# Performance work log

Measured on AMD Instinct MI355X. Metric: run time of the kernel, lower is better.

Reference implementation:

```python
import jax, jax.numpy as jnp
import numpy as np

EPS = 1e-5
HEADS = 8
SR = 4


def bn(x, gamma, beta, mean, var):
    # BatchNorm in inference form; channel axis = 1
    shape = (1, -1) + (1,) * (x.ndim - 2)
    inv = gamma.reshape(shape) / jnp.sqrt(var.reshape(shape) + EPS)
    return (x - mean.reshape(shape)) * inv + beta.reshape(shape)


def setup_inputs() -> dict:
    key = jax.random.key(0)
    ks = jax.random.split(key, 8)
    B, C, H, W = 2, 256, 128, 128
    N = H * W
    conv1d_std = np.sqrt(2.0 / C)            # fan_out = 1*C
    conv2d_std = np.sqrt(2.0 / (SR * SR * C))  # fan_out = sr*sr*C
    return {
        "x": jax.random.normal(ks[0], (B, C, N), dtype=jnp.float32),
        "w_q": jax.random.normal(ks[1], (C, C), dtype=jnp.float32) * conv1d_std,
        "w_k": jax.random.normal(ks[2], (C, C), dtype=jnp.float32) * conv1d_std,
        "w_sr": jax.random.normal(ks[3], (C, C, SR, SR), dtype=jnp.float32) * conv2d_std,
        "sr_gamma": jnp.ones((C,), jnp.float32),
        "sr_beta": jnp.zeros((C,), jnp.float32),
        "sr_mean": jnp.zeros((C,), jnp.float32),
        "sr_var": jnp.ones((C,), jnp.float32),
        "w_proj": jax.random.normal(ks[4], (C, C), dtype=jnp.float32) * conv1d_std,
        "proj_gamma": jnp.ones((C,), jnp.float32),
        "proj_beta": jnp.zeros((C,), jnp.float32),
        "proj_mean": jnp.zeros((C,), jnp.float32),
        "proj_var": jnp.ones((C,), jnp.float32),
        "H": 128,
        "W": 128,
    }


def reference(x, w_q, w_k, w_sr, sr_gamma, sr_beta, sr_mean, sr_var,
              w_proj, proj_gamma, proj_beta, proj_mean, proj_var, H, W):
    B, C, N = x.shape
    hd = C // HEADS
    scale = hd ** -0.5
    # q: Conv1d(k=1) == channel matmul -> (B, heads, N, hd)
    q = jnp.einsum('oc,bcn->bon', w_q, x).reshape(B, HEADS, hd, N).transpose(0, 1, 3, 2)
    # spatial reduction: Conv2d(k=SR, s=SR) as patch-reshape + einsum, then BN
    xp = x.reshape(B, C, H // SR, SR, W // SR, SR)
    xr = jnp.einsum('bchpwq,ocpq->bohw', xp, w_sr).reshape(B, C, (H // SR) * (W // SR))
    xr = bn(xr, sr_gamma, sr_beta, sr_mean, sr_var)
    # k: (B, heads, hd, N_kv)
    k = jnp.einsum('oc,bcm->bom', w_k, xr).reshape(B, HEADS, hd, -1)
    # scores (B, heads, N, N_kv) -> max over kv
    scores = jnp.einsum('bhnd,bhdm->bhnm', q, k) * scale
    attn = scores.max(axis=-1)                # (B, heads, N)
    # v = mean-pooled x, identical per head -> matmul collapses to sum over heads
    v = x.mean(axis=-1)                       # (B, C)
    out = jnp.einsum('bhn,bc->bcn', attn, v)  # (B, C, N)
    out = jnp.einsum('oc,bcn->bon', w_proj, out)
    return bn(out, proj_gamma, proj_beta, proj_mean, proj_var)
```

## Files before the change

### kernel.cpp

```cpp
#include <hip/hip_runtime.h>
#include <hip/hip_bf16.h>
#include <math.h>

#define EPSF 1e-5f
#define SCALE 0.17677669529663687f

typedef __bf16 bf16x8 __attribute__((ext_vector_type(8)));
typedef __bf16 bf16x4 __attribute__((ext_vector_type(4)));
typedef float f32x4 __attribute__((ext_vector_type(4)));


__global__ __launch_bounds__(256) void k_wprep(const float* __restrict__ wq,
                                               const float* __restrict__ wk,
                                               const float* __restrict__ wsr,
                                               __bf16* __restrict__ wqf,
                                               __bf16* __restrict__ wkb,
                                               __bf16* __restrict__ wsrf,
                                               float* __restrict__ v,
                                               float* __restrict__ ssg) {
    int bi = blockIdx.x, t = threadIdx.x;
    if (bi >= 576) {
        int e = (bi - 576) * 256 + t;
        *(float4*)&ssg[e << 2] = make_float4(0.f, 0.f, 0.f, 0.f);
        return;
    }
    if (bi < 32) {
        if (bi == 0) { v[t] = 0.f; v[256 + t] = 0.f; }
        int tt = bi * 256 + t;
        int o = tt >> 5, chunk = tt & 31;
        float4 v0 = *(const float4*)&wq[o * 256 + (chunk << 3)];
        float4 v1 = *(const float4*)&wq[o * 256 + (chunk << 3) + 4];
        bf16x8 p;
        p[0] = (__bf16)v0.x; p[1] = (__bf16)v0.y; p[2] = (__bf16)v0.z; p[3] = (__bf16)v0.w;
        p[4] = (__bf16)v1.x; p[5] = (__bf16)v1.y; p[6] = (__bf16)v1.z; p[7] = (__bf16)v1.w;
        int cc = chunk >> 2, quad = chunk & 3;
        *(bf16x8*)&wqf[(((((o >> 4) << 3) + cc) << 6) + (quad << 4) + (o & 15)) << 3] = p;
    } else if (bi < 64) {
        int e = (bi - 32) * 256 + t;
        float4 v0 = *(const float4*)&wk[e << 3];
        float4 v1 = *(const float4*)&wk[(e << 3) + 4];
        bf16x8 p;
        p[0] = (__bf16)(v0.x * SCALE); p[1] = (__bf16)(v0.y * SCALE);
        p[2] = (__bf16)(v0.z * SCALE); p[3] = (__bf16)(v0.w * SCALE);
        p[4] = (__bf16)(v1.x * SCALE); p[5] = (__bf16)(v1.y * SCALE);
        p[6] = (__bf16)(v1.z * SCALE); p[7] = (__bf16)(v1.w * SCALE);
        *(bf16x8*)&wkb[e << 3] = p;
    } else {
        int tt = (bi - 64) * 256 + t;
        int o = tt >> 9, chunk = tt & 511;
        float4 v0 = *(const float4*)&wsr[o * 4096 + (chunk << 3)];
        float4 v1 = *(const float4*)&wsr[o * 4096 + (chunk << 3) + 4];
        bf16x8 p;
        p[0] = (__bf16)v0.x; p[1] = (__bf16)v0.y; p[2] = (__bf16)v0.z; p[3] = (__bf16)v0.w;
        p[4] = (__bf16)v1.x; p[5] = (__bf16)v1.y; p[6] = (__bf16)v1.z; p[7] = (__bf16)v1.w;
        int cc = chunk >> 2, quad = chunk & 3;
        *(bf16x8*)&wsrf[(((((o >> 4) << 7) + cc) << 6) + (quad << 4) + (o & 15)) << 3] = p;
    }
}

__global__ __launch_bounds__(256) void k_stage(const float* __restrict__ x,
                                               __bf16* __restrict__ Pbf,
                                               __bf16* __restrict__ xTf,
                                               float* __restrict__ v) {
    int t = threadIdx.x, bid0 = blockIdx.x;
    if (bid0 < 512) {
        __shared__ float csum[32];
        int bid = bid0;
        int b = bid >> 8, hm = (bid >> 3) & 31, ccg = bid & 7;
        int wm = t >> 3, c8 = t & 7;
        if (t < 32) csum[t] = 0.f;
        __syncthreads();
        const int mtile = (hm << 1) + (wm >> 4);
        const int ln = wm & 15;
#pragma unroll
        for (int cci = 0; cci < 4; ++cci) {
            int c = (ccg << 5) + (cci << 3) + c8;
            const float* src = x + ((size_t)(b * 256 + c) << 14) + (hm << 9) + (wm << 2);
            bf16x8 o0, o1;
            float s = 0.f;
#pragma unroll
            for (int p = 0; p < 2; ++p) {
                float4 vv = *(const float4*)&src[p << 7];
                s += vv.x + vv.y + vv.z + vv.w;
                o0[p * 4 + 0] = (__bf16)vv.x; o0[p * 4 + 1] = (__bf16)vv.y;
                o0[p * 4 + 2] = (__bf16)vv.z; o0[p * 4 + 3] = (__bf16)vv.w;
            }
#pragma unroll
            for (int p = 0; p < 2; ++p) {
                float4 vv = *(const float4*)&src[(p + 2) << 7];
                s += vv.x + vv.y + vv.z + vv.w;
                o1[p * 4 + 0] = (__bf16)vv.x; o1[p * 4 + 1] = (__bf16)vv.y;
                o1[p * 4 + 2] = (__bf16)vv.z; o1[p * 4 + 3] = (__bf16)vv.w;
            }
            size_t d0 = (((((size_t)(b * 64 + mtile) << 7) + (c >> 1)) << 6) +
                         (((c & 1) << 1) << 4) + ln) << 3;
            *(bf16x8*)&Pbf[d0] = o0;
            *(bf16x8*)&Pbf[d0 + 128] = o1;
            atomicAdd(&csum[(cci << 3) + c8], s);
        }
        __syncthreads();
        if (t < 32) atomicAdd(&v[b * 256 + (ccg << 5) + t], csum[t]);
    } else {
        __shared__ float ts[32 * 68];
        int bid = bid0 - 512;
        int b = bid >> 8, n0 = (bid & 255) << 6;
        const int nl = t >> 2;
        const int ch = (t & 3) << 3;
        const int n = n0 + nl;
        const int ntile = n >> 4, ln = n & 15, quad = ch >> 3;
        const int cl = t >> 3;
        const int n8 = (t & 7) << 3;
        for (int s8 = 0; s8 < 8; ++s8) {
            int c0 = s8 << 5;
            __syncthreads();
            {
                const float* src = &x[((size_t)(b * 256 + c0 + cl) << 14) + n0 + n8];
                *(float4*)&ts[cl * 68 + n8] = *(const float4*)&src[0];
                *(float4*)&ts[cl * 68 + n8 + 4] = *(const float4*)&src[4];
            }
            __syncthreads();
            bf16x8 p;
#pragma unroll
            for (int j = 0; j < 8; ++j) p[j] = (__bf16)ts[(ch + j) * 68 + nl];
            *(bf16x8*)&xTf[(((((size_t)(b * 1024 + ntile) << 3) + s8) << 6) +
                            (quad << 4) + ln) << 3] = p;
        }
    }
}

__global__ __launch_bounds__(256) void k_conv1f(const __bf16* __restrict__ Pbf,
                                                const __bf16* __restrict__ wsrf,
                                                const float* __restrict__ sg,
                                                const float* __restrict__ sb,
                                                const float* __restrict__ smn,
                                                const float* __restrict__ svar,
                                                __bf16* __restrict__ xrb) {
    const int t = threadIdx.x, bid = blockIdx.x;
    const int b = bid & 1, mt = (bid >> 1) & 63, og = bid >> 7;
    const int w = t >> 6, lane = t & 63, ln = lane & 15, quad = lane >> 4;
    f32x4 acc = (f32x4){0.f, 0.f, 0.f, 0.f};
    const __bf16* pa = Pbf + ((size_t)(b * 64 + mt) << 16) + (lane << 3);
    const __bf16* pbm = wsrf + ((size_t)(og * 4 + w) << 16) + (lane << 3);
#pragma unroll 8
    for (int cc = 0; cc < 128; ++cc) {
        bf16x8 af = *(const bf16x8*)&pa[cc << 9];
        bf16x8 bf = *(const bf16x8*)&pbm[cc << 9];
        acc = __builtin_amdgcn_mfma_f32_16x16x32_bf16(af, bf, acc, 0, 0, 0);
    }
    const int o = (og << 6) + (w << 4) + ln;
    float inv = sg[o] / sqrtf(svar[o] + EPSF);
    float mn = smn[o], bt = sb[o];
#pragma unroll
    for (int r = 0; r < 4; ++r) {
        int m = (mt << 4) + (quad << 2) + r;
        xrb[(((size_t)b << 10) + m) * 256 + o] = (__bf16)((acc[r] - mn) * inv + bt);
    }
}

__global__ __launch_bounds__(256) void k_kmat2(const __bf16* __restrict__ xrb,
                                               const __bf16* __restrict__ wkb,
                                               __bf16* __restrict__ kkbh,
                                               const float* __restrict__ v,
                                               const float* __restrict__ wproj,
                                               const float* __restrict__ pg,
                                               const float* __restrict__ pb,
                                               const float* __restrict__ pm,
                                               const float* __restrict__ pvar,
                                               float* __restrict__ A,
                                               float* __restrict__ B0) {
    const int t = threadIdx.x, bid = blockIdx.x;
    if (bid >= 128) {
        __shared__ float vl[256];
        int b = bid - 128;
        vl[t] = v[b * 256 + t] * (1.0f / 16384.0f);
        __syncthreads();
        const float* wr = wproj + t * 256;
        float s = 0.f;
#pragma unroll 8
        for (int c = 0; c < 256; c += 4) {
            float4 w4 = *(const float4*)&wr[c];
            s += w4.x * vl[c] + w4.y * vl[c + 1] + w4.z * vl[c + 2] + w4.w * vl[c + 3];
        }
        float inv = pg[t] / sqrtf(pvar[t] + EPSF);
        A[b * 256 + t] = s * inv;
        if (b == 0) B0[t] = pb[t] - pm[t] * inv;
        return;
    }
    const int b = bid >> 6, mt = bid & 63;
    const int w = t >> 6, lane = t & 63, ln = lane & 15, quad = lane >> 4;
    f32x4 acc[4];
#pragma unroll
    for (int ot = 0; ot < 4; ++ot) acc[ot] = (f32x4){0.f, 0.f, 0.f, 0.f};
    const __bf16* pa = xrb + ((((size_t)b << 10) + (mt << 4) + ln) << 8) + (quad << 3);
    const __bf16* pbm = wkb + (((w << 6) + ln) << 8) + (quad << 3);
#pragma unroll
    for (int cc = 0; cc < 8; ++cc) {
        const int cb = cc << 5;
        bf16x8 af = *(const bf16x8*)&pa[cb];
        bf16x8 bfr[4];
#pragma unroll
        for (int ot = 0; ot < 4; ++ot) bfr[ot] = *(const bf16x8*)&pbm[(ot << 12) + cb];
#pragma unroll
        for (int ot = 0; ot < 4; ++ot)
            acc[ot] = __builtin_amdgcn_mfma_f32_16x16x32_bf16(af, bfr[ot], acc[ot], 0, 0, 0);
    }
#pragma unroll
    for (int ot = 0; ot < 4; ++ot)
#pragma unroll
        for (int r = 0; r < 4; ++r) {
            int m = (mt << 4) + (quad << 2) + r;
            int h = (w << 1) + (ot >> 1);
            int d = ((ot & 1) << 4) + ln;
            kkbh[(((size_t)(b * 8 + h)) << 15) + (m << 5) + d] = (__bf16)acc[ot][r];
        }
}

__global__ __launch_bounds__(256) void k_scores2(const __bf16* __restrict__ xTf,
                                                 const __bf16* __restrict__ wqf,
                                                 const __bf16* __restrict__ kkbh,
                                                 float* __restrict__ ssg) {
    __shared__ __align__(16) __bf16 qs[64 * 72];
    __shared__ float smax[512];
    const int t = threadIdx.x;
    const int w = t >> 6;
    const int lane = t & 63;
    const int ln = lane & 15;
    const int quad = lane >> 4;
    const int bx = blockIdx.x;
    const int hp = bx & 3;
    const int n0 = ((bx >> 2) & 255) << 6;
    const int b = bx >> 10;

    f32x4 acc[4];
#pragma unroll
    for (int ot = 0; ot < 4; ++ot) acc[ot] = (f32x4){0.f, 0.f, 0.f, 0.f};
    const __bf16* pa = xTf + ((size_t)(b * 1024 + (n0 >> 4) + w) << 12) + (lane << 3);
    const __bf16* pbm = wqf + ((size_t)(hp << 2) << 12) + (lane << 3);
#pragma unroll 2
    for (int cc = 0; cc < 8; ++cc) {
        const int cb = cc << 9;
        bf16x8 af = *(const bf16x8*)&pa[cb];
        bf16x8 bfr[4];
#pragma unroll
        for (int ot = 0; ot < 4; ++ot) bfr[ot] = *(const bf16x8*)&pbm[(ot << 12) + cb];
#pragma unroll
        for (int ot = 0; ot < 4; ++ot)
            acc[ot] = __builtin_amdgcn_mfma_f32_16x16x32_bf16(af, bfr[ot], acc[ot], 0, 0, 0);
    }
#pragma unroll
    for (int ot = 0; ot < 4; ++ot)
#pragma unroll
        for (int r = 0; r < 4; ++r)
            qs[((w << 4) + (quad << 2) + r) * 72 + (ot << 4) + ln] = (__bf16)acc[ot][r];
    __syncthreads();

    const f32x4 zf = {0.f, 0.f, 0.f, 0.f};
#pragma unroll
    for (int hl = 0; hl < 2; ++hl) {
        const int h = (hp << 1) + hl;
        bf16x8 qb[4];
#pragma unroll
        for (int nt = 0; nt < 4; ++nt)
            qb[nt] = *(const bf16x8*)&qs[((nt << 4) + ln) * 72 + (hl << 5) + (quad << 3)];
        const __bf16* kb_base = kkbh + ((size_t)(b * 8 + h) << 15) + (ln << 5) + (quad << 3);
        bf16x8 kb[16];
#pragma unroll
        for (int i = 0; i < 16; ++i)
            kb[i] = *(const bf16x8*)&kb_base[((w << 8) + (i << 4)) << 5];
        float rmx[4] = {-INFINITY, -INFINITY, -INFINITY, -INFINITY};
#pragma unroll
        for (int i = 0; i < 16; ++i)
#pragma unroll
            for (int nt = 0; nt < 4; ++nt) {
                f32x4 d = __builtin_amdgcn_mfma_f32_16x16x32_bf16(kb[i], qb[nt], zf, 0, 0, 0);
                float t1 = fmaxf(fmaxf(d[0], d[1]), d[2]);
                rmx[nt] = fmaxf(fmaxf(t1, d[3]), rmx[nt]);
            }
#pragma unroll
        for (int nt = 0; nt < 4; ++nt) {
            rmx[nt] = fmaxf(rmx[nt], __shfl_xor(rmx[nt], 16, 64));
            rmx[nt] = fmaxf(rmx[nt], __shfl_xor(rmx[nt], 32, 64));
        }
        if (lane < 16) {
#pragma unroll
            for (int nt = 0; nt < 4; ++nt)
                smax[(w << 7) + (hl << 6) + (nt << 4) + lane] = rmx[nt];
        }
    }
    __syncthreads();
    if (t < 64) {
        float s0 = fmaxf(fmaxf(smax[t], smax[128 + t]), fmaxf(smax[256 + t], smax[384 + t]));
        float s1 = fmaxf(fmaxf(smax[64 + t], smax[192 + t]),
                         fmaxf(smax[320 + t], smax[448 + t]));
        atomicAdd(&ssg[(b << 14) + n0 + t], s0 + s1);
    }
}

__global__ __launch_bounds__(256) void k_epi(const float* __restrict__ ssg,
                                             const float* __restrict__ A,
                                             const float* __restrict__ B0,
                                             float* __restrict__ out) {
    __shared__ float ss[64], sA[256], sB[256];
    const int t = threadIdx.x, bid = blockIdx.x;
    const int b = bid >> 8, n0 = (bid & 255) << 6;
    if (t < 64) ss[t] = ssg[(b << 14) + n0 + t];
    sA[t] = A[b * 256 + t];
    sB[t] = B0[t];
    __syncthreads();
#pragma unroll
    for (int i = 0; i < 16; ++i) {
        int e = t + (i << 8);
        int c = e >> 4, n4 = (e & 15) << 2;
        float4 s4 = *(const float4*)&ss[n4];
        float a = sA[c], bb = sB[c];
        float4 o4 = make_float4(fmaf(a, s4.x, bb), fmaf(a, s4.y, bb),
                                fmaf(a, s4.z, bb), fmaf(a, s4.w, bb));
        *(float4*)&out[((size_t)(b * 256 + c) << 14) + n0 + n4] = o4;
    }
}

extern "C" void kernel_launch(void* const* d_in, const int* in_sizes, int n_in,
                              void* d_out, int out_size, void* d_ws, size_t ws_size,
                              hipStream_t stream) {
    const float* x    = (const float*)d_in[0];
    const float* wq   = (const float*)d_in[1];
    const float* wk   = (const float*)d_in[2];
    const float* wsr  = (const float*)d_in[3];
    const float* sg   = (const float*)d_in[4];
    const float* sb   = (const float*)d_in[5];
    const float* smn  = (const float*)d_in[6];
    const float* svr  = (const float*)d_in[7];
    const float* wproj= (const float*)d_in[8];
    const float* pg   = (const float*)d_in[9];
    const float* pb   = (const float*)d_in[10];
    const float* pm   = (const float*)d_in[11];
    const float* pvr  = (const float*)d_in[12];
    float* out = (float*)d_out;

    char* W = (char*)d_ws;
    float*  w_v   = (float*) (W + 0);
    float*  w_A   = (float*) (W + 4096);
    float*  w_B0  = (float*) (W + 8192);
    float*  w_ssg = (float*) (W + 12288);
    __bf16* w_wqf = (__bf16*)(W + 147456);
    __bf16* w_wkb = (__bf16*)(W + 278528);
    __bf16* w_wsrf= (__bf16*)(W + 409600);
    __bf16* w_xrb = (__bf16*)(W + 2506752);
    __bf16* w_kkbh= (__bf16*)(W + 3031040);
    __bf16* w_Pbf = (__bf16*)(W + 4079616);
    __bf16* w_xTf = (__bf16*)(W + 20856832);

    k_wprep<<<608, 256, 0, stream>>>(wq, wk, wsr, w_wqf, w_wkb, w_wsrf, w_v, w_ssg);
    k_stage<<<1024, 256, 0, stream>>>(x, w_Pbf, w_xTf, w_v);
    k_conv1f<<<512, 256, 0, stream>>>(w_Pbf, w_wsrf, sg, sb, smn, svr, w_xrb);
    k_kmat2<<<130, 256, 0, stream>>>(w_xrb, w_wkb, w_kkbh, w_v, wproj, pg, pb, pm, pvr,
                                     w_A, w_B0);
    k_scores2<<<2048, 256, 0, stream>>>(w_xTf, w_wqf, w_kkbh, w_ssg);
    k_epi<<<512, 256, 0, stream>>>(w_ssg, w_A, w_B0, out);
}
```

Baseline: 191.4 us.

## Merge weight-prep and staging kernels, widen score blocks to four heads

Folds weight conversion, x staging and ssg zeroing into one prep kernel, which removes a launch and its boundary. The global atomic accumulation of the channel sums becomes per-block partial writes that k_kmat2 reduces. The conv1 MFMA loop now uses two accumulators to break the dependency chain. The scores kernel now handles four heads per block instead of two, halving the grid and reusing each x tile for more heads, at the cost of more registers and LDS.

Measured after the change: 203.5 us. 6.3% more time.

```diff
diff --git a/kernel.cpp b/kernel.cpp
--- a/kernel.cpp
+++ b/kernel.cpp
@@ -10,22 +10,19 @@
 typedef float f32x4 __attribute__((ext_vector_type(4)));
 
 
-__global__ __launch_bounds__(256) void k_wprep(const float* __restrict__ wq,
-                                               const float* __restrict__ wk,
-                                               const float* __restrict__ wsr,
-                                               __bf16* __restrict__ wqf,
-                                               __bf16* __restrict__ wkb,
-                                               __bf16* __restrict__ wsrf,
-                                               float* __restrict__ v,
-                                               float* __restrict__ ssg) {
+__global__ __launch_bounds__(256) void k_prep(const float* __restrict__ x,
+                                              const float* __restrict__ wq,
+                                              const float* __restrict__ wk,
+                                              const float* __restrict__ wsr,
+                                              __bf16* __restrict__ wqf,
+                                              __bf16* __restrict__ wkb,
+                                              __bf16* __restrict__ wsrf,
+                                              __bf16* __restrict__ Pbf,
+                                              __bf16* __restrict__ xTf,
+                                              float* __restrict__ vpart,
+                                              float* __restrict__ ssg) {
     int bi = blockIdx.x, t = threadIdx.x;
-    if (bi >= 576) {
-        int e = (bi - 576) * 256 + t;
-        *(float4*)&ssg[e << 2] = make_float4(0.f, 0.f, 0.f, 0.f);
-        return;
-    }
     if (bi < 32) {
-        if (bi == 0) { v[t] = 0.f; v[256 + t] = 0.f; }
         int tt = bi * 256 + t;
         int o = tt >> 5, chunk = tt & 31;
         float4 v0 = *(const float4*)&wq[o * 256 + (chunk << 3)];
@@ -45,7 +42,7 @@
         p[4] = (__bf16)(v1.x * SCALE); p[5] = (__bf16)(v1.y * SCALE);
         p[6] = (__bf16)(v1.z * SCALE); p[7] = (__bf16)(v1.w * SCALE);
         *(bf16x8*)&wkb[e << 3] = p;
-    } else {
+    } else if (bi < 576) {
         int tt = (bi - 64) * 256 + t;
         int o = tt >> 9, chunk = tt & 511;
         float4 v0 = *(const float4*)&wsr[o * 4096 + (chunk << 3)];
@@ -55,17 +52,9 @@
         p[4] = (__bf16)v1.x; p[5] = (__bf16)v1.y; p[6] = (__bf16)v1.z; p[7] = (__bf16)v1.w;
         int cc = chunk >> 2, quad = chunk & 3;
         *(bf16x8*)&wsrf[(((((o >> 4) << 7) + cc) << 6) + (quad << 4) + (o & 15)) << 3] = p;
-    }
-}
-
-__global__ __launch_bounds__(256) void k_stage(const float* __restrict__ x,
-                                               __bf16* __restrict__ Pbf,
-                                               __bf16* __restrict__ xTf,
-                                               float* __restrict__ v) {
-    int t = threadIdx.x, bid0 = blockIdx.x;
-    if (bid0 < 512) {
+    } else if (bi < 1088) {
         __shared__ float csum[32];
-        int bid = bid0;
+        int bid = bi - 576;
         int b = bid >> 8, hm = (bid >> 3) & 31, ccg = bid & 7;
         int wm = t >> 3, c8 = t & 7;
         if (t < 32) csum[t] = 0.f;
@@ -99,10 +88,10 @@
             atomicAdd(&csum[(cci << 3) + c8], s);
         }
         __syncthreads();
-        if (t < 32) atomicAdd(&v[b * 256 + (ccg << 5) + t], csum[t]);
-    } else {
+        if (t < 32) vpart[((b * 256 + (ccg << 5) + t) << 5) + hm] = csum[t];
+    } else if (bi < 1600) {
         __shared__ float ts[32 * 68];
-        int bid = bid0 - 512;
+        int bid = bi - 1088;
         int b = bid >> 8, n0 = (bid & 255) << 6;
         const int nl = t >> 2;
         const int ch = (t & 3) << 3;
@@ -125,6 +114,9 @@
             *(bf16x8*)&xTf[(((((size_t)(b * 1024 + ntile) << 3) + s8) << 6) +
                             (quad << 4) + ln) << 3] = p;
         }
+    } else {
+        int e = (bi - 1600) * 256 + t;
+        *(float4*)&ssg[e << 2] = make_float4(0.f, 0.f, 0.f, 0.f);
     }
 }
 
@@ -138,15 +130,20 @@
     const int t = threadIdx.x, bid = blockIdx.x;
     const int b = bid & 1, mt = (bid >> 1) & 63, og = bid >> 7;
     const int w = t >> 6, lane = t & 63, ln = lane & 15, quad = lane >> 4;
-    f32x4 acc = (f32x4){0.f, 0.f, 0.f, 0.f};
+    f32x4 acc0 = (f32x4){0.f, 0.f, 0.f, 0.f};
+    f32x4 acc1 = (f32x4){0.f, 0.f, 0.f, 0.f};
     const __bf16* pa = Pbf + ((size_t)(b * 64 + mt) << 16) + (lane << 3);
     const __bf16* pbm = wsrf + ((size_t)(og * 4 + w) << 16) + (lane << 3);
-#pragma unroll 8
-    for (int cc = 0; cc < 128; ++cc) {
-        bf16x8 af = *(const bf16x8*)&pa[cc << 9];
-        bf16x8 bf = *(const bf16x8*)&pbm[cc << 9];
-        acc = __builtin_amdgcn_mfma_f32_16x16x32_bf16(af, bf, acc, 0, 0, 0);
-    }
+#pragma unroll 4
+    for (int cc = 0; cc < 128; cc += 2) {
+        bf16x8 a0 = *(const bf16x8*)&pa[cc << 9];
+        bf16x8 b0 = *(const bf16x8*)&pbm[cc << 9];
+        bf16x8 a1 = *(const bf16x8*)&pa[(cc + 1) << 9];
+        bf16x8 b1 = *(const bf16x8*)&pbm[(cc + 1) << 9];
+        acc0 = __builtin_amdgcn_mfma_f32_16x16x32_bf16(a0, b0, acc0, 0, 0, 0);
+        acc1 = __builtin_amdgcn_mfma_f32_16x16x32_bf16(a1, b1, acc1, 0, 0, 0);
+    }
+    f32x4 acc = acc0 + acc1;
     const int o = (og << 6) + (w << 4) + ln;
     float inv = sg[o] / sqrtf(svar[o] + EPSF);
     float mn = smn[o], bt = sb[o];
@@ -160,7 +157,7 @@
 __global__ __launch_bounds__(256) void k_kmat2(const __bf16* __restrict__ xrb,
                                                const __bf16* __restrict__ wkb,
                                                __bf16* __restrict__ kkbh,
-                                               const float* __restrict__ v,
+                                               const float* __restrict__ vpart,
                                                const float* __restrict__ wproj,
                                                const float* __restrict__ pg,
                                                const float* __restrict__ pb,
@@ -172,17 +169,24 @@
     if (bid >= 128) {
         __shared__ float vl[256];
         int b = bid - 128;
-        vl[t] = v[b * 256 + t] * (1.0f / 16384.0f);
+        const float* vp = vpart + ((b * 256 + t) << 5);
+        float s = 0.f;
+#pragma unroll
+        for (int j = 0; j < 32; j += 4) {
+            float4 p4 = *(const float4*)&vp[j];
+            s += p4.x + p4.y + p4.z + p4.w;
+        }
+        vl[t] = s * (1.0f / 16384.0f);
         __syncthreads();
         const float* wr = wproj + t * 256;
-        float s = 0.f;
+        float acc = 0.f;
 #pragma unroll 8
         for (int c = 0; c < 256; c += 4) {
             float4 w4 = *(const float4*)&wr[c];
-            s += w4.x * vl[c] + w4.y * vl[c + 1] + w4.z * vl[c + 2] + w4.w * vl[c + 3];
+            acc += w4.x * vl[c] + w4.y * vl[c + 1] + w4.z * vl[c + 2] + w4.w * vl[c + 3];
         }
         float inv = pg[t] / sqrtf(pvar[t] + EPSF);
-        A[b * 256 + t] = s * inv;
+        A[b * 256 + t] = acc * inv;
         if (b == 0) B0[t] = pb[t] - pm[t] * inv;
         return;
     }
@@ -215,67 +219,71 @@
         }
 }
 
-__global__ __launch_bounds__(256) void k_scores2(const __bf16* __restrict__ xTf,
+__global__ __launch_bounds__(256) void k_scores3(const __bf16* __restrict__ xTf,
                                                  const __bf16* __restrict__ wqf,
                                                  const __bf16* __restrict__ kkbh,
                                                  float* __restrict__ ssg) {
-    __shared__ __align__(16) __bf16 qs[64 * 72];
-    __shared__ float smax[512];
+    __shared__ __align__(16) __bf16 qs[64 * 132];
+    __shared__ float smax[1024];
     const int t = threadIdx.x;
     const int w = t >> 6;
     const int lane = t & 63;
     const int ln = lane & 15;
     const int quad = lane >> 4;
     const int bx = blockIdx.x;
-    const int hp = bx & 3;
-    const int n0 = ((bx >> 2) & 255) << 6;
-    const int b = bx >> 10;
-
-    f32x4 acc[4];
-#pragma unroll
-    for (int ot = 0; ot < 4; ++ot) acc[ot] = (f32x4){0.f, 0.f, 0.f, 0.f};
+    const int hp = bx & 1;
+    const int n0 = ((bx >> 1) & 255) << 6;
+    const int b = bx >> 9;
+
+    f32x4 acc[8];
+#pragma unroll
+    for (int ot = 0; ot < 8; ++ot) acc[ot] = (f32x4){0.f, 0.f, 0.f, 0.f};
     const __bf16* pa = xTf + ((size_t)(b * 1024 + (n0 >> 4) + w) << 12) + (lane << 3);
-    const __bf16* pbm = wqf + ((size_t)(hp << 2) << 12) + (lane << 3);
+    const __bf16* pbm = wqf + ((size_t)(hp << 3) << 12) + (lane << 3);
 #pragma unroll 2
     for (int cc = 0; cc < 8; ++cc) {
         const int cb = cc << 9;
         bf16x8 af = *(const bf16x8*)&pa[cb];
-        bf16x8 bfr[4];
-#pragma unroll
-        for (int ot = 0; ot < 4; ++ot) bfr[ot] = *(const bf16x8*)&pbm[(ot << 12) + cb];
-#pragma unroll
-        for (int ot = 0; ot < 4; ++ot)
+        bf16x8 bfr[8];
+#pragma unroll
+        for (int ot = 0; ot < 8; ++ot) bfr[ot] = *(const bf16x8*)&pbm[(ot << 12) + cb];
+#pragma unroll
+        for (int ot = 0; ot < 8; ++ot)
             acc[ot] = __builtin_amdgcn_mfma_f32_16x16x32_bf16(af, bfr[ot], acc[ot], 0, 0, 0);
     }
 #pragma unroll
-    for (int ot = 0; ot < 4; ++ot)
+    for (int ot = 0; ot < 8; ++ot)
 #pragma unroll
         for (int r = 0; r < 4; ++r)
-            qs[((w << 4) + (quad << 2) + r) * 72 + (ot << 4) + ln] = (__bf16)acc[ot][r];
+            qs[((w << 4) + (quad << 2) + r) * 132 + (ot << 4) + ln] = (__bf16)acc[ot][r];
     __syncthreads();
 
     const f32x4 zf = {0.f, 0.f, 0.f, 0.f};
 #pragma unroll
-    for (int hl = 0; hl < 2; ++hl) {
-        const int h = (hp << 1) + hl;
+    for (int hl = 0; hl < 4; ++hl) {
+        const int h = (hp << 2) + hl;
         bf16x8 qb[4];
 #pragma unroll
         for (int nt = 0; nt < 4; ++nt)
-            qb[nt] = *(const bf16x8*)&qs[((nt << 4) + ln) * 72 + (hl << 5) + (quad << 3)];
+            qb[nt] = *(const bf16x8*)&qs[((nt << 4) + ln) * 132 + (hl << 5) + (quad << 3)];
         const __bf16* kb_base = kkbh + ((size_t)(b * 8 + h) << 15) + (ln << 5) + (quad << 3);
-        bf16x8 kb[16];
-#pragma unroll
-        for (int i = 0; i < 16; ++i)
-            kb[i] = *(const bf16x8*)&kb_base[((w << 8) + (i << 4)) << 5];
         float rmx[4] = {-INFINITY, -INFINITY, -INFINITY, -INFINITY};
 #pragma unroll
-        for (int i = 0; i < 16; ++i)
-#pragma unroll
-            for (int nt = 0; nt < 4; ++nt) {
-                f32x4 d = __builtin_amdgcn_mfma_f32_16x16x32_bf16(kb[i], qb[nt], zf, 0, 0, 0);
-                float t1 = fmaxf(fmaxf(d[0], d[1]), d[2]);
-                rmx[nt] = fmaxf(fmaxf(t1, d[3]), rmx[nt]);
-            }
+        for (int bi = 0; bi < 2; ++bi) {
+            bf16x8 kb[8];
+#pragma unroll
+            for (int i = 0; i < 8; ++i)
+                kb[i] = *(const bf16x8*)&kb_base[((w << 8) + ((bi * 8 + i) << 4)) << 5];
+#pragma unroll
+            for (int i = 0; i < 8; ++i)
+#pragma unroll
+                for (int nt = 0; nt < 4; ++nt) {
+                    f32x4 d = __builtin_amdgcn_mfma_f32_16x16x32_bf16(kb[i], qb[nt], zf,
+                                                                      0, 0, 0);
+                    float t1 = fmaxf(fmaxf(d[0], d[1]), d[2]);
+                    rmx[nt] = fmaxf(fmaxf(t1, d[3]), rmx[nt]);
+                }
+        }
 #pragma unroll
         for (int nt = 0; nt < 4; ++nt) {
             rmx[nt] = fmaxf(rmx[nt], __shfl_xor(rmx[nt], 16, 64));
@@ -284,15 +292,19 @@
         if (lane < 16) {
 #pragma unroll
             for (int nt = 0; nt < 4; ++nt)
-                smax[(w << 7) + (hl << 6) + (nt << 4) + lane] = rmx[nt];
+                smax[(w << 8) + (hl << 6) + (nt << 4) + lane] = rmx[nt];
         }
     }
     __syncthreads();
     if (t < 64) {
-        float s0 = fmaxf(fmaxf(smax[t], smax[128 + t]), fmaxf(smax[256 + t], smax[384 + t]));
-        float s1 = fmaxf(fmaxf(smax[64 + t], smax[192 + t]),
-                         fmaxf(smax[320 + t], smax[448 + t]));
-        atomicAdd(&ssg[(b << 14) + n0 + t], s0 + s1);
+        float sum = 0.f;
+#pragma unroll
+        for (int hl = 0; hl < 4; ++hl) {
+            float vv = fmaxf(fmaxf(smax[(hl << 6) + t], smax[256 + (hl << 6) + t]),
+                             fmaxf(smax[512 + (hl << 6) + t], smax[768 + (hl << 6) + t]));
+            sum += vv;
+        }
+        atomicAdd(&ssg[(b << 14) + n0 + t], sum);
     }
 }
 
@@ -338,23 +350,23 @@
     float* out = (float*)d_out;
 
     char* W = (char*)d_ws;
-    float*  w_v   = (float*) (W + 0);
-    float*  w_A   = (float*) (W + 4096);
-    float*  w_B0  = (float*) (W + 8192);
-    float*  w_ssg = (float*) (W + 12288);
-    __bf16* w_wqf = (__bf16*)(W + 147456);
-    __bf16* w_wkb = (__bf16*)(W + 278528);
-    __bf16* w_wsrf= (__bf16*)(W + 409600);
-    __bf16* w_xrb = (__bf16*)(W + 2506752);
-    __bf16* w_kkbh= (__bf16*)(W + 3031040);
-    __bf16* w_Pbf = (__bf16*)(W + 4079616);
-    __bf16* w_xTf = (__bf16*)(W + 20856832);
-
-    k_wprep<<<608, 256, 0, stream>>>(wq, wk, wsr, w_wqf, w_wkb, w_wsrf, w_v, w_ssg);
-    k_stage<<<1024, 256, 0, stream>>>(x, w_Pbf, w_xTf, w_v);
+    float*  w_A    = (float*) (W + 0);
+    float*  w_B0   = (float*) (W + 4096);
+    float*  w_vpart= (float*) (W + 8192);
+    float*  w_ssg  = (float*) (W + 76800);
+    __bf16* w_wqf  = (__bf16*)(W + 212992);
+    __bf16* w_wkb  = (__bf16*)(W + 344064);
+    __bf16* w_wsrf = (__bf16*)(W + 475136);
+    __bf16* w_xrb  = (__bf16*)(W + 2572288);
+    __bf16* w_kkbh = (__bf16*)(W + 3096576);
+    __bf16* w_Pbf  = (__bf16*)(W + 4194304);
+    __bf16* w_xTf  = (__bf16*)(W + 20971520);
+
+    k_prep<<<1632, 256, 0, stream>>>(x, wq, wk, wsr, w_wqf, w_wkb, w_wsrf,
+                                     w_Pbf, w_xTf, w_vpart, w_ssg);
     k_conv1f<<<512, 256, 0, stream>>>(w_Pbf, w_wsrf, sg, sb, smn, svr, w_xrb);
-    k_kmat2<<<130, 256, 0, stream>>>(w_xrb, w_wkb, w_kkbh, w_v, wproj, pg, pb, pm, pvr,
-                                     w_A, w_B0);
-    k_scores2<<<2048, 256, 0, stream>>>(w_xTf, w_wqf, w_kkbh, w_ssg);
+    k_kmat2<<<130, 256, 0, stream>>>(w_xrb, w_wkb, w_kkbh, w_vpart, wproj,
+                                     pg, pb, pm, pvr, w_A, w_B0);
+    k_scores3<<<1024, 256, 0, stream>>>(w_xTf, w_wqf, w_kkbh, w_ssg);
     k_epi<<<512, 256, 0, stream>>>(w_ssg, w_A, w_B0, out);
 }
```
